# Kernel optimization log

Hardware: AMD Instinct MI355X
Metric: run time of the kernel (lower is better)

Reference implementation:

```python
import jax, jax.numpy as jnp
import numpy as np

B, C, Q, E = 32, 1024, 128, 512

def setup_inputs() -> dict:
    key = jax.random.key(0)
    k1, k2, k3 = jax.random.split(key, 3)
    context = jax.random.normal(k1, (B, C, E), dtype=jnp.float32)
    question = jax.random.normal(k2, (B, Q, E), dtype=jnp.float32)
    # ws = [ws_q | ws_c | ws_m], matching cat([q, ctx, q*ctx]) order
    ws = jax.random.normal(k3, (3 * E,), dtype=jnp.float32) * (1.0 / np.sqrt(E))
    return {"context": context, "question": question, "ws": ws}

def reference(context, question, ws):
    ws_q, ws_c, ws_m = ws[:E], ws[E:2 * E], ws[2 * E:]
    # similarity[b,c,q] = ws_q.q[b,q] + ws_c.c[b,c] + ws_m.(q[b,q]*c[b,c])
    sim = (jnp.einsum('bqe,e->bq', question, ws_q)[:, None, :]
           + jnp.einsum('bce,e->bc', context, ws_c)[:, :, None]
           + jnp.einsum('bce,bqe,e->bcq', context, question, ws_m))  # (B,C,Q)
    c2q = jnp.einsum('bcq,bqe->bce', jax.nn.softmax(sim, axis=2), question)  # (B,C,E)
    q2c_w = jax.nn.softmax(jnp.max(sim, axis=2), axis=1)  # (B,C)
    q2c = jnp.einsum('bc,bce->be', q2c_w, context)[:, None, :]  # (B,1,E)
    return (c2q, q2c)
```

## Files before the change

### kernel.cpp

```cpp
#include <hip/hip_runtime.h>

#define BB 32
#define CC 1024
#define QQ 128
#define EE 512

typedef unsigned int uint32;
typedef unsigned short u16;
typedef __bf16 bf16x8 __attribute__((ext_vector_type(8)));
typedef float f32x4 __attribute__((ext_vector_type(4)));

#define QMF_OFF  (0u)
#define QTF_OFF  (4u<<20)
#define PV_OFF   (8u<<20)
#define QD_OFF   (12u<<20)
#define MT_OFF   ((12u<<20) + 16384u)
#define ST_OFF   (MT_OFF + 8192u)

__device__ __forceinline__ u16 bfc(float f){
  __bf16 h = (__bf16)f;
  return __builtin_bit_cast(u16, h);
}
__device__ __forceinline__ float bf2f(uint32 lo16){
  return __builtin_bit_cast(float, lo16 << 16);
}

__global__ __launch_bounds__(256) void k_prep_qm(const float* __restrict__ q,
                                                 const float* __restrict__ ws,
                                                 unsigned char* __restrict__ wsp){
  const int b = blockIdx.x >> 2, et = blockIdx.x & 3, e0 = et*128;
  __shared__ u16 tile[128*136];
  const int tid = threadIdx.x;
  #pragma unroll
  for (int i=0;i<16;i++){
    int id = tid + i*256;
    int qi = id >> 5;
    int el = (id & 31) << 2;
    float4 v = *(const float4*)(q + (size_t)(b*QQ+qi)*EE + e0 + el);
    float4 m = *(const float4*)(ws + 2*EE + e0 + el);
    float4 c = *(const float4*)(ws +   EE + e0 + el);
    ushort4 u; u.x = bfc(v.x*m.x + c.x); u.y = bfc(v.y*m.y + c.y);
               u.z = bfc(v.z*m.z + c.z); u.w = bfc(v.w*m.w + c.w);
    *(ushort4*)&tile[qi*136 + el] = u;
  }
  __syncthreads();
  const int lane = tid & 63, wv = tid >> 6, l15 = lane & 15, l4 = lane >> 4;
  uint4* qmf = (uint4*)(wsp + QMF_OFF);
  #pragma unroll
  for (int i=0;i<8;i++){
    int f = wv*8 + i;
    int kl = f >> 3, nf = f & 7;
    uint4 u = *(const uint4*)&tile[(nf*16 + l15)*136 + kl*32 + l4*8];
    qmf[(size_t)((b*16 + et*4 + kl)*8 + nf)*64 + lane] = u;
  }
}

__global__ __launch_bounds__(256) void k_prep_qt(const float* __restrict__ q,
                                                 unsigned char* __restrict__ wsp){
  const int b = blockIdx.x >> 2, et = blockIdx.x & 3, e0 = et*128;
  __shared__ u16 tile[128*136];
  const int tid = threadIdx.x;
  #pragma unroll
  for (int i=0;i<16;i++){
    int id = tid + i*256;
    int qi = id >> 5;
    int el = (id & 31) << 2;
    float4 v = *(const float4*)(q + (size_t)(b*QQ+qi)*EE + e0 + el);
    ushort4 u; u.x = bfc(v.x); u.y = bfc(v.y); u.z = bfc(v.z); u.w = bfc(v.w);
    *(ushort4*)&tile[qi*136 + el] = u;
  }
  __syncthreads();
  const int lane = tid & 63, wv = tid >> 6, l15 = lane & 15, l4 = lane >> 4;
  uint4* qtf = (uint4*)(wsp + QTF_OFF);
  #pragma unroll
  for (int i=0;i<8;i++){
    int f = wv*8 + i;
    int ks2 = f >> 3, nl = f & 7, ne = et*8 + nl;
    uint32 x[4];
    #pragma unroll
    for (int p=0;p<4;p++){
      u16 t0 = tile[(ks2*32 + l4*8 + 2*p    )*136 + nl*16 + l15];
      u16 t1 = tile[(ks2*32 + l4*8 + 2*p + 1)*136 + nl*16 + l15];
      x[p] = (uint32)t0 | ((uint32)t1 << 16);
    }
    uint4 u; u.x = x[0]; u.y = x[1]; u.z = x[2]; u.w = x[3];
    qtf[(size_t)((b*4 + ks2)*32 + ne)*64 + lane] = u;
  }
}

__global__ __launch_bounds__(256) void k_prep_qd(const float* __restrict__ q,
                                                 const float* __restrict__ ws,
                                                 unsigned char* __restrict__ wsp){
  const int row = blockIdx.x*4 + (threadIdx.x >> 6);
  const int lane = threadIdx.x & 63;
  const float4* qr = (const float4*)(q + (size_t)row*EE) + lane*2;
  const float4* wq = (const float4*)ws + lane*2;
  float4 v0 = qr[0], v1 = qr[1], a0 = wq[0], a1 = wq[1];
  float dot = v0.x*a0.x + v0.y*a0.y + v0.z*a0.z + v0.w*a0.w
            + v1.x*a1.x + v1.y*a1.y + v1.z*a1.z + v1.w*a1.w;
  #pragma unroll
  for (int off=1; off<64; off<<=1) dot += __shfl_xor(dot, off);
  if (lane == 0) ((float*)(wsp + QD_OFF))[row] = dot;
}

__global__ __attribute__((amdgpu_flat_work_group_size(512, 512)))
           __attribute__((amdgpu_waves_per_eu(4, 4)))
void k_main(const float* __restrict__ ctx,
            unsigned char* __restrict__ wsp,
            float* __restrict__ out){
  __shared__ __align__(16) unsigned char tile[65536];
  __shared__ __align__(16) float mx_s[64*8];
  __shared__ __align__(16) float sm_s[64*8];
  __shared__ float wrow_s[4][16];

  const int bid = blockIdx.x;
  const int sw  = (bid & 7)*64 + (bid >> 3);
  const int b   = sw >> 4;
  const int t   = sw & 15;
  const int tid = threadIdx.x;
  const int lane = tid & 63;
  const int w    = tid >> 6;
  const int l15  = lane & 15;
  const int l4   = lane >> 4;
  const int rg   = w >> 1;
  const int eh   = w & 1;

  const float4* cb4 = (const float4*)(ctx + (size_t)(b*CC + t*64)*EE);
  {
    float4 v[16];
    #pragma unroll
    for (int i=0;i<16;i++) v[i] = cb4[i*512 + tid];
    const int colb = (tid & 127)*8;
    #pragma unroll
    for (int i=0;i<16;i++){
      int row = i*4 + (tid >> 7);
      uint2 u;
      u.x = (uint32)bfc(v[i].x) | ((uint32)bfc(v[i].y) << 16);
      u.y = (uint32)bfc(v[i].z) | ((uint32)bfc(v[i].w) << 16);
      *(uint2*)(tile + row*1024 + (colb ^ ((row & 7) << 4))) = u;
    }
  }
  const uint4* qmf4 = (const uint4*)(wsp + QMF_OFF);
  bf16x8 a[16];
  #pragma unroll
  for (int ks=0; ks<16; ks++)
    a[ks] = __builtin_bit_cast(bf16x8, qmf4[(size_t)((b*16 + ks)*8 + w)*64 + lane]);
  const float4 qdv = *(const float4*)((const float*)(wsp + QD_OFF) + b*QQ + w*16 + l4*4);
  __syncthreads();

  f32x4 acc[4];
  #pragma unroll
  for (int cc=0;cc<4;cc++) acc[cc] = (f32x4){0.f,0.f,0.f,0.f};
  #pragma unroll
  for (int ks=0; ks<16; ks++){
    #pragma unroll
    for (int cc=0; cc<4; cc++){
      const int row = cc*16 + l15;
      bf16x8 bf = __builtin_bit_cast(bf16x8,
        *(const uint4*)(tile + row*1024 + ((ks*64 + l4*16) ^ ((row & 7) << 4))));
      acc[cc] = __builtin_amdgcn_mfma_f32_16x16x32_bf16(a[ks], bf, acc[cc], 0, 0, 0);
    }
  }
  __syncthreads();

  {
    float pm[4], ps[4];
    #pragma unroll
    for (int cc=0; cc<4; cc++){
      float m = -3.0e38f, s = 0.f;
      u16 hb[4];
      #pragma unroll
      for (int r=0;r<4;r++){
        float vv = acc[cc][r] + qdv[r];
        vv = fminf(vv, 80.f);
        m = fmaxf(m, vv);
        u16 h = bfc(__expf(vv));
        hb[r] = h;
        s += bf2f(h);
      }
      uint2 u; u.x = (uint32)hb[0] | ((uint32)hb[1]<<16);
               u.y = (uint32)hb[2] | ((uint32)hb[3]<<16);
      *(uint2*)(tile + (cc*4 + (w>>1))*1024 + (((w&1)*2 + (l4>>1))*16 + l15)*16 + (l4&1)*8) = u;
      m = fmaxf(m, __shfl_xor(m, 16)); m = fmaxf(m, __shfl_xor(m, 32));
      s += __shfl_xor(s, 16);          s += __shfl_xor(s, 32);
      pm[cc] = m; ps[cc] = s;
    }
    if (l4 == 0){
      #pragma unroll
      for (int cc=0; cc<4; cc++){
        mx_s[(cc*16 + l15)*8 + w] = pm[cc];
        sm_s[(cc*16 + l15)*8 + w] = ps[cc];
      }
    }
  }
  __syncthreads();

  float rden[4];
  #pragma unroll
  for (int r=0;r<4;r++){
    const int c = rg*16 + l4*4 + r;
    f32x4 s0 = *(const f32x4*)&sm_s[c*8];
    f32x4 s1 = *(const f32x4*)&sm_s[c*8 + 4];
    rden[r] = 1.f/(s0[0]+s0[1]+s0[2]+s0[3]+s1[0]+s1[1]+s1[2]+s1[3]);
  }

  if (eh == 0){
    float mf[4];
    #pragma unroll
    for (int r=0;r<4;r++){
      const int c = rg*16 + l4*4 + r;
      f32x4 m0 = *(const f32x4*)&mx_s[c*8];
      f32x4 m1 = *(const f32x4*)&mx_s[c*8 + 4];
      mf[r] = fmaxf(fmaxf(fmaxf(m0[0],m0[1]), fmaxf(m0[2],m0[3])),
                    fmaxf(fmaxf(m1[0],m1[1]), fmaxf(m1[2],m1[3])));
    }
    float m16 = fmaxf(fmaxf(mf[0],mf[1]), fmaxf(mf[2],mf[3]));
    m16 = fmaxf(m16, __shfl_xor(m16, 16));
    m16 = fmaxf(m16, __shfl_xor(m16, 32));
    float wr[4], s16 = 0.f;
    #pragma unroll
    for (int r=0;r<4;r++){ wr[r] = __expf(mf[r] - m16); s16 += wr[r]; }
    s16 += __shfl_xor(s16, 16);
    s16 += __shfl_xor(s16, 32);
    if (l15 == 0){
      #pragma unroll
      for (int r=0;r<4;r++) wrow_s[rg][l4*4 + r] = wr[r];
    }
    if (lane == 0){
      ((float*)(wsp + MT_OFF))[b*64 + t*4 + rg] = m16;
      ((float*)(wsp + ST_OFF))[b*64 + t*4 + rg] = s16;
    }
  }

  bf16x8 pa[4];
  #pragma unroll
  for (int k2=0;k2<4;k2++)
    pa[k2] = __builtin_bit_cast(bf16x8, *(const uint4*)(tile + (rg*4 + k2)*1024 + lane*16));

  unsigned char* qstage = tile + 16384;
  const unsigned char* qtfb = wsp + QTF_OFF + (size_t)b*131072;
  auto dma = [&](int p){
    #pragma unroll
    for (int j=0;j<2;j++){
      const int f = w*2 + j;
      const int ks2 = f >> 2, nl = f & 3;
      const unsigned char* g = qtfb + (size_t)(ks2*32 + p*4 + nl)*1024 + lane*16;
      __builtin_amdgcn_global_load_lds(
        (const __attribute__((address_space(1))) uint32*)g,
        (__attribute__((address_space(3))) uint32*)(qstage + (p&1)*16384 + f*1024),
        16, 0, 0);
    }
  };
  dma(0);
  __syncthreads();

  float* ob = out + (size_t)(b*CC + t*64 + rg*16)*EE;
  #pragma unroll
  for (int p=0; p<8; p++){
    if (p < 7) dma(p+1);
    const unsigned char* qs = qstage + (p&1)*16384;
    f32x4 ac0 = (f32x4){0.f,0.f,0.f,0.f};
    f32x4 ac1 = (f32x4){0.f,0.f,0.f,0.f};
    #pragma unroll
    for (int k2=0;k2<4;k2++){
      bf16x8 b0 = __builtin_bit_cast(bf16x8, *(const uint4*)(qs + (k2*4 + eh*2 + 0)*1024 + lane*16));
      bf16x8 b1 = __builtin_bit_cast(bf16x8, *(const uint4*)(qs + (k2*4 + eh*2 + 1)*1024 + lane*16));
      ac0 = __builtin_amdgcn_mfma_f32_16x16x32_bf16(pa[k2], b0, ac0, 0, 0, 0);
      ac1 = __builtin_amdgcn_mfma_f32_16x16x32_bf16(pa[k2], b1, ac1, 0, 0, 0);
    }
    #pragma unroll
    for (int r=0;r<4;r++){
      ob[(size_t)(l4*4 + r)*EE + p*64 + eh*32 +  0 + l15] = ac0[r]*rden[r];
      ob[(size_t)(l4*4 + r)*EE + p*64 + eh*32 + 16 + l15] = ac1[r]*rden[r];
    }
    __syncthreads();
  }

  {
    const float4* cq = (const float4*)(ctx + (size_t)(b*CC + t*64 + rg*16)*EE + eh*256) + lane;
    float4 a4; a4.x = 0.f; a4.y = 0.f; a4.z = 0.f; a4.w = 0.f;
    #pragma unroll
    for (int rr=0; rr<16; rr++){
      float wv = wrow_s[rg][rr];
      float4 g = cq[(size_t)rr*128];
      a4.x = fmaf(wv, g.x, a4.x); a4.y = fmaf(wv, g.y, a4.y);
      a4.z = fmaf(wv, g.z, a4.z); a4.w = fmaf(wv, g.w, a4.w);
    }
    float* pv = (float*)(wsp + PV_OFF) + (size_t)(b*64 + t*4 + rg)*EE + eh*256 + lane*4;
    *(float4*)pv = a4;
  }
}

__global__ __launch_bounds__(256) void k_fin(unsigned char* __restrict__ wsp,
                                             float* __restrict__ out){
  const int b = blockIdx.x;
  __shared__ float sc_s[64];
  const int tid = threadIdx.x;
  if (tid < 64){
    float Mg = ((const float*)(wsp + MT_OFF))[b*64 + tid];
    float Sg = ((const float*)(wsp + ST_OFF))[b*64 + tid];
    float M = Mg;
    #pragma unroll
    for (int off=1; off<64; off<<=1) M = fmaxf(M, __shfl_xor(M, off));
    float ev = __expf(Mg - M);
    float ds = ev * Sg;
    #pragma unroll
    for (int off=1; off<64; off<<=1) ds += __shfl_xor(ds, off);
    sc_s[tid] = ev / ds;
  }
  __syncthreads();
  const float* pv = (const float*)(wsp + PV_OFF) + (size_t)b*64*EE;
  float a0 = 0.f, a1 = 0.f;
  #pragma unroll 8
  for (int g=0; g<64; g++){
    float s = sc_s[g];
    a0 = fmaf(s, pv[g*EE + tid],       a0);
    a1 = fmaf(s, pv[g*EE + tid + 256], a1);
  }
  size_t base = (size_t)BB*CC*EE + (size_t)b*EE;
  out[base + tid]       = a0;
  out[base + tid + 256] = a1;
}

extern "C" void kernel_launch(void* const* d_in, const int* in_sizes, int n_in,
                              void* d_out, int out_size, void* d_ws, size_t ws_size,
                              hipStream_t stream){
  const float* ctx = (const float*)d_in[0];
  const float* q   = (const float*)d_in[1];
  const float* ws  = (const float*)d_in[2];
  float* out = (float*)d_out;
  unsigned char* wsp = (unsigned char*)d_ws;

  k_prep_qm<<<dim3(BB*4),    dim3(256), 0, stream>>>(q, ws, wsp);
  k_prep_qt<<<dim3(BB*4),    dim3(256), 0, stream>>>(q, wsp);
  k_prep_qd<<<dim3(BB*QQ/4), dim3(256), 0, stream>>>(q, ws, wsp);
  k_main   <<<dim3(512),     dim3(512), 0, stream>>>(ctx, wsp, out);
  k_fin    <<<dim3(BB),      dim3(256), 0, stream>>>(wsp, out);
}
```

Before: 58.58 us.

## Merge prep kernels and process two context tiles per main block

The three question-preprocessing kernels are fused into one that emits the bf16 QM and QT fragments plus per-slice partial q·ws_q dots in a single pass over the question. The main kernel now handles two 64-row context tiles per block with double-buffered LDS (128KB). It prefetches the second tile's context during the first tile's GEMM and softmax, and reuses each staged QT chunk for both tiles in the c2q GEMM. This removes two launches and halves QT staging traffic. In exchange the grid drops to 256 blocks, occupancy falls (waves_per_eu 2, larger LDS), and register pressure rises.

```diff
diff --git a/kernel.cpp b/kernel.cpp
--- a/kernel.cpp
+++ b/kernel.cpp
@@ -13,8 +13,8 @@
 #define QMF_OFF  (0u)
 #define QTF_OFF  (4u<<20)
 #define PV_OFF   (8u<<20)
-#define QD_OFF   (12u<<20)
-#define MT_OFF   ((12u<<20) + 16384u)
+#define QDP_OFF  (12u<<20)
+#define MT_OFF   ((12u<<20) + 65536u)
 #define ST_OFF   (MT_OFF + 8192u)
 
 __device__ __forceinline__ u16 bfc(float f){
@@ -25,53 +25,44 @@
   return __builtin_bit_cast(float, lo16 << 16);
 }
 
-__global__ __launch_bounds__(256) void k_prep_qm(const float* __restrict__ q,
-                                                 const float* __restrict__ ws,
-                                                 unsigned char* __restrict__ wsp){
+__global__ __launch_bounds__(256) void k_prep(const float* __restrict__ q,
+                                              const float* __restrict__ ws,
+                                              unsigned char* __restrict__ wsp){
   const int b = blockIdx.x >> 2, et = blockIdx.x & 3, e0 = et*128;
-  __shared__ u16 tile[128*136];
+  __shared__ u16 tm[128*136];
+  __shared__ u16 tt[128*136];
   const int tid = threadIdx.x;
+  float* qdp = (float*)(wsp + QDP_OFF) + (size_t)(b*4 + et)*128;
   #pragma unroll
   for (int i=0;i<16;i++){
     int id = tid + i*256;
     int qi = id >> 5;
     int el = (id & 31) << 2;
     float4 v = *(const float4*)(q + (size_t)(b*QQ+qi)*EE + e0 + el);
-    float4 m = *(const float4*)(ws + 2*EE + e0 + el);
-    float4 c = *(const float4*)(ws +   EE + e0 + el);
-    ushort4 u; u.x = bfc(v.x*m.x + c.x); u.y = bfc(v.y*m.y + c.y);
-               u.z = bfc(v.z*m.z + c.z); u.w = bfc(v.w*m.w + c.w);
-    *(ushort4*)&tile[qi*136 + el] = u;
+    float4 a = *(const float4*)(ws +          e0 + el);
+    float4 c = *(const float4*)(ws +   EE +   e0 + el);
+    float4 m = *(const float4*)(ws + 2*EE +   e0 + el);
+    ushort4 um; um.x = bfc(v.x*m.x + c.x); um.y = bfc(v.y*m.y + c.y);
+                um.z = bfc(v.z*m.z + c.z); um.w = bfc(v.w*m.w + c.w);
+    *(ushort4*)&tm[qi*136 + el] = um;
+    ushort4 ut; ut.x = bfc(v.x); ut.y = bfc(v.y); ut.z = bfc(v.z); ut.w = bfc(v.w);
+    *(ushort4*)&tt[qi*136 + el] = ut;
+    float d = v.x*a.x + v.y*a.y + v.z*a.z + v.w*a.w;
+    d += __shfl_xor(d,1); d += __shfl_xor(d,2); d += __shfl_xor(d,4);
+    d += __shfl_xor(d,8); d += __shfl_xor(d,16);
+    if ((tid & 31) == 0) qdp[qi] = d;
   }
   __syncthreads();
   const int lane = tid & 63, wv = tid >> 6, l15 = lane & 15, l4 = lane >> 4;
   uint4* qmf = (uint4*)(wsp + QMF_OFF);
+  uint4* qtf = (uint4*)(wsp + QTF_OFF);
   #pragma unroll
   for (int i=0;i<8;i++){
     int f = wv*8 + i;
     int kl = f >> 3, nf = f & 7;
-    uint4 u = *(const uint4*)&tile[(nf*16 + l15)*136 + kl*32 + l4*8];
+    uint4 u = *(const uint4*)&tm[(nf*16 + l15)*136 + kl*32 + l4*8];
     qmf[(size_t)((b*16 + et*4 + kl)*8 + nf)*64 + lane] = u;
   }
-}
-
-__global__ __launch_bounds__(256) void k_prep_qt(const float* __restrict__ q,
-                                                 unsigned char* __restrict__ wsp){
-  const int b = blockIdx.x >> 2, et = blockIdx.x & 3, e0 = et*128;
-  __shared__ u16 tile[128*136];
-  const int tid = threadIdx.x;
-  #pragma unroll
-  for (int i=0;i<16;i++){
-    int id = tid + i*256;
-    int qi = id >> 5;
-    int el = (id & 31) << 2;
-    float4 v = *(const float4*)(q + (size_t)(b*QQ+qi)*EE + e0 + el);
-    ushort4 u; u.x = bfc(v.x); u.y = bfc(v.y); u.z = bfc(v.z); u.w = bfc(v.w);
-    *(ushort4*)&tile[qi*136 + el] = u;
-  }
-  __syncthreads();
-  const int lane = tid & 63, wv = tid >> 6, l15 = lane & 15, l4 = lane >> 4;
-  uint4* qtf = (uint4*)(wsp + QTF_OFF);
   #pragma unroll
   for (int i=0;i<8;i++){
     int f = wv*8 + i;
@@ -79,8 +70,8 @@
     uint32 x[4];
     #pragma unroll
     for (int p=0;p<4;p++){
-      u16 t0 = tile[(ks2*32 + l4*8 + 2*p    )*136 + nl*16 + l15];
-      u16 t1 = tile[(ks2*32 + l4*8 + 2*p + 1)*136 + nl*16 + l15];
+      u16 t0 = tt[(ks2*32 + l4*8 + 2*p    )*136 + nl*16 + l15];
+      u16 t1 = tt[(ks2*32 + l4*8 + 2*p + 1)*136 + nl*16 + l15];
       x[p] = (uint32)t0 | ((uint32)t1 << 16);
     }
     uint4 u; u.x = x[0]; u.y = x[1]; u.z = x[2]; u.w = x[3];
@@ -88,35 +79,21 @@
   }
 }
 
-__global__ __launch_bounds__(256) void k_prep_qd(const float* __restrict__ q,
-                                                 const float* __restrict__ ws,
-                                                 unsigned char* __restrict__ wsp){
-  const int row = blockIdx.x*4 + (threadIdx.x >> 6);
-  const int lane = threadIdx.x & 63;
-  const float4* qr = (const float4*)(q + (size_t)row*EE) + lane*2;
-  const float4* wq = (const float4*)ws + lane*2;
-  float4 v0 = qr[0], v1 = qr[1], a0 = wq[0], a1 = wq[1];
-  float dot = v0.x*a0.x + v0.y*a0.y + v0.z*a0.z + v0.w*a0.w
-            + v1.x*a1.x + v1.y*a1.y + v1.z*a1.z + v1.w*a1.w;
-  #pragma unroll
-  for (int off=1; off<64; off<<=1) dot += __shfl_xor(dot, off);
-  if (lane == 0) ((float*)(wsp + QD_OFF))[row] = dot;
-}
-
 __global__ __attribute__((amdgpu_flat_work_group_size(512, 512)))
-           __attribute__((amdgpu_waves_per_eu(4, 4)))
+           __attribute__((amdgpu_waves_per_eu(2)))
 void k_main(const float* __restrict__ ctx,
             unsigned char* __restrict__ wsp,
             float* __restrict__ out){
-  __shared__ __align__(16) unsigned char tile[65536];
-  __shared__ __align__(16) float mx_s[64*8];
-  __shared__ __align__(16) float sm_s[64*8];
-  __shared__ float wrow_s[4][16];
+  __shared__ __align__(16) unsigned char buf[2][65536];
+  __shared__ __align__(16) float mxA[2][64*8];
+  __shared__ __align__(16) float smA[2][64*8];
+  __shared__ float wrowA[2][4][16];
 
   const int bid = blockIdx.x;
-  const int sw  = (bid & 7)*64 + (bid >> 3);
-  const int b   = sw >> 4;
-  const int t   = sw & 15;
+  const int sw  = (bid & 7)*32 + (bid >> 3);
+  const int b   = sw >> 3;
+  const int pr  = sw & 7;
+  const int t0  = pr*2, t1 = pr*2 + 1;
   const int tid = threadIdx.x;
   const int lane = tid & 63;
   const int w    = tid >> 6;
@@ -125,53 +102,71 @@
   const int rg   = w >> 1;
   const int eh   = w & 1;
 
-  const float4* cb4 = (const float4*)(ctx + (size_t)(b*CC + t*64)*EE);
+  const float4* cb0 = (const float4*)(ctx + (size_t)(b*CC + t0*64)*EE);
+  const float4* cb1 = (const float4*)(ctx + (size_t)(b*CC + t1*64)*EE);
+  float4 v[16];
+  #pragma unroll
+  for (int i=0;i<16;i++) v[i] = cb0[i*512 + tid];
+
+  const uint4* qmf4 = (const uint4*)(wsp + QMF_OFF);
+  bf16x8 a[16];
+  #pragma unroll
+  for (int ks=0; ks<16; ks++)
+    a[ks] = __builtin_bit_cast(bf16x8, qmf4[(size_t)((b*16 + ks)*8 + w)*64 + lane]);
+  float qdv[4];
   {
-    float4 v[16];
-    #pragma unroll
-    for (int i=0;i<16;i++) v[i] = cb4[i*512 + tid];
-    const int colb = (tid & 127)*8;
+    const float* qdp = (const float*)(wsp + QDP_OFF) + (size_t)b*512;
+    #pragma unroll
+    for (int r=0;r<4;r++){
+      const int qi = w*16 + l4*4 + r;
+      qdv[r] = qdp[qi] + qdp[128+qi] + qdp[256+qi] + qdp[384+qi];
+    }
+  }
+
+  const int colb = (tid & 127)*8;
+  auto stage_write = [&](unsigned char* dst){
     #pragma unroll
     for (int i=0;i<16;i++){
       int row = i*4 + (tid >> 7);
       uint2 u;
       u.x = (uint32)bfc(v[i].x) | ((uint32)bfc(v[i].y) << 16);
       u.y = (uint32)bfc(v[i].z) | ((uint32)bfc(v[i].w) << 16);
-      *(uint2*)(tile + row*1024 + (colb ^ ((row & 7) << 4))) = u;
-    }
-  }
-  const uint4* qmf4 = (const uint4*)(wsp + QMF_OFF);
-  bf16x8 a[16];
-  #pragma unroll
-  for (int ks=0; ks<16; ks++)
-    a[ks] = __builtin_bit_cast(bf16x8, qmf4[(size_t)((b*16 + ks)*8 + w)*64 + lane]);
-  const float4 qdv = *(const float4*)((const float*)(wsp + QD_OFF) + b*QQ + w*16 + l4*4);
-  __syncthreads();
-
+      *(uint2*)(dst + row*1024 + (colb ^ ((row & 7) << 4))) = u;
+    }
+  };
+
+  stage_write(buf[0]);
+  __syncthreads();
+
+  #pragma unroll
+  for (int i=0;i<16;i++) v[i] = cb1[i*512 + tid];
+
+  auto gemm1 = [&](const unsigned char* bp, f32x4* acc){
+    #pragma unroll
+    for (int cc=0;cc<4;cc++) acc[cc] = (f32x4){0.f,0.f,0.f,0.f};
+    #pragma unroll
+    for (int ks=0; ks<16; ks++){
+      #pragma unroll
+      for (int cc=0; cc<4; cc++){
+        const int row = cc*16 + l15;
+        bf16x8 bf = __builtin_bit_cast(bf16x8,
+          *(const uint4*)(bp + row*1024 + ((ks*64 + l4*16) ^ ((row & 7) << 4))));
+        acc[cc] = __builtin_amdgcn_mfma_f32_16x16x32_bf16(a[ks], bf, acc[cc], 0, 0, 0);
+      }
+    }
+  };
   f32x4 acc[4];
-  #pragma unroll
-  for (int cc=0;cc<4;cc++) acc[cc] = (f32x4){0.f,0.f,0.f,0.f};
-  #pragma unroll
-  for (int ks=0; ks<16; ks++){
-    #pragma unroll
-    for (int cc=0; cc<4; cc++){
-      const int row = cc*16 + l15;
-      bf16x8 bf = __builtin_bit_cast(bf16x8,
-        *(const uint4*)(tile + row*1024 + ((ks*64 + l4*16) ^ ((row & 7) << 4))));
-      acc[cc] = __builtin_amdgcn_mfma_f32_16x16x32_bf16(a[ks], bf, acc[cc], 0, 0, 0);
-    }
-  }
-  __syncthreads();
-
-  {
-    float pm[4], ps[4];
+  gemm1(buf[0], acc);
+  __syncthreads();
+
+  auto softmax = [&](int ti, f32x4* ac){
     #pragma unroll
     for (int cc=0; cc<4; cc++){
       float m = -3.0e38f, s = 0.f;
       u16 hb[4];
       #pragma unroll
       for (int r=0;r<4;r++){
-        float vv = acc[cc][r] + qdv[r];
+        float vv = ac[cc][r] + qdv[r];
         vv = fminf(vv, 80.f);
         m = fmaxf(m, vv);
         u16 h = bfc(__expf(vv));
@@ -180,37 +175,36 @@
       }
       uint2 u; u.x = (uint32)hb[0] | ((uint32)hb[1]<<16);
                u.y = (uint32)hb[2] | ((uint32)hb[3]<<16);
-      *(uint2*)(tile + (cc*4 + (w>>1))*1024 + (((w&1)*2 + (l4>>1))*16 + l15)*16 + (l4&1)*8) = u;
+      *(uint2*)(buf[ti] + (cc*4 + (w>>1))*1024 + (((w&1)*2 + (l4>>1))*16 + l15)*16 + (l4&1)*8) = u;
       m = fmaxf(m, __shfl_xor(m, 16)); m = fmaxf(m, __shfl_xor(m, 32));
       s += __shfl_xor(s, 16);          s += __shfl_xor(s, 32);
-      pm[cc] = m; ps[cc] = s;
-    }
-    if (l4 == 0){
-      #pragma unroll
-      for (int cc=0; cc<4; cc++){
-        mx_s[(cc*16 + l15)*8 + w] = pm[cc];
-        sm_s[(cc*16 + l15)*8 + w] = ps[cc];
+      if (l4 == 0){
+        mxA[ti][(cc*16 + l15)*8 + w] = m;
+        smA[ti][(cc*16 + l15)*8 + w] = s;
       }
     }
-  }
-  __syncthreads();
-
-  float rden[4];
-  #pragma unroll
-  for (int r=0;r<4;r++){
-    const int c = rg*16 + l4*4 + r;
-    f32x4 s0 = *(const f32x4*)&sm_s[c*8];
-    f32x4 s1 = *(const f32x4*)&sm_s[c*8 + 4];
-    rden[r] = 1.f/(s0[0]+s0[1]+s0[2]+s0[3]+s1[0]+s1[1]+s1[2]+s1[3]);
-  }
-
-  if (eh == 0){
-    float mf[4];
+  };
+  softmax(0, acc);
+  stage_write(buf[1]);
+  __syncthreads();
+
+  auto rden_of = [&](int ti, float* rd){
     #pragma unroll
     for (int r=0;r<4;r++){
       const int c = rg*16 + l4*4 + r;
-      f32x4 m0 = *(const f32x4*)&mx_s[c*8];
-      f32x4 m1 = *(const f32x4*)&mx_s[c*8 + 4];
+      f32x4 s0 = *(const f32x4*)&smA[ti][c*8];
+      f32x4 s1 = *(const f32x4*)&smA[ti][c*8 + 4];
+      rd[r] = 1.f/(s0[0]+s0[1]+s0[2]+s0[3]+s1[0]+s1[1]+s1[2]+s1[3]);
+    }
+  };
+  auto q2c_stats = [&](int ti, int tglob){
+    if (eh != 0) return;
+    float mf[4];
+    #pragma unroll
+    for (int r=0;r<4;r++){
+      const int c = rg*16 + l4*4 + r;
+      f32x4 m0 = *(const f32x4*)&mxA[ti][c*8];
+      f32x4 m1 = *(const f32x4*)&mxA[ti][c*8 + 4];
       mf[r] = fmaxf(fmaxf(fmaxf(m0[0],m0[1]), fmaxf(m0[2],m0[3])),
                     fmaxf(fmaxf(m1[0],m1[1]), fmaxf(m1[2],m1[3])));
     }
@@ -224,20 +218,23 @@
     s16 += __shfl_xor(s16, 32);
     if (l15 == 0){
       #pragma unroll
-      for (int r=0;r<4;r++) wrow_s[rg][l4*4 + r] = wr[r];
+      for (int r=0;r<4;r++) wrowA[ti][rg][l4*4 + r] = wr[r];
     }
     if (lane == 0){
-      ((float*)(wsp + MT_OFF))[b*64 + t*4 + rg] = m16;
-      ((float*)(wsp + ST_OFF))[b*64 + t*4 + rg] = s16;
-    }
-  }
-
-  bf16x8 pa[4];
+      ((float*)(wsp + MT_OFF))[b*64 + tglob*4 + rg] = m16;
+      ((float*)(wsp + ST_OFF))[b*64 + tglob*4 + rg] = s16;
+    }
+  };
+
+  float rden0[4], rden1[4];
+  rden_of(0, rden0);
+  q2c_stats(0, t0);
+  bf16x8 pa0[4], pa1[4];
   #pragma unroll
   for (int k2=0;k2<4;k2++)
-    pa[k2] = __builtin_bit_cast(bf16x8, *(const uint4*)(tile + (rg*4 + k2)*1024 + lane*16));
-
-  unsigned char* qstage = tile + 16384;
+    pa0[k2] = __builtin_bit_cast(bf16x8, *(const uint4*)(buf[0] + (rg*4 + k2)*1024 + lane*16));
+
+  unsigned char* qstage = buf[0] + 16384;
   const unsigned char* qtfb = wsp + QTF_OFF + (size_t)b*131072;
   auto dma = [&](int p){
     #pragma unroll
@@ -252,41 +249,60 @@
     }
   };
   dma(0);
-  __syncthreads();
-
-  float* ob = out + (size_t)(b*CC + t*64 + rg*16)*EE;
+
+  gemm1(buf[1], acc);
+  __syncthreads();
+  softmax(1, acc);
+  __syncthreads();
+  rden_of(1, rden1);
+  q2c_stats(1, t1);
+  #pragma unroll
+  for (int k2=0;k2<4;k2++)
+    pa1[k2] = __builtin_bit_cast(bf16x8, *(const uint4*)(buf[1] + (rg*4 + k2)*1024 + lane*16));
+
+  float* ob0 = out + (size_t)(b*CC + t0*64 + rg*16)*EE;
+  float* ob1 = out + (size_t)(b*CC + t1*64 + rg*16)*EE;
   #pragma unroll
   for (int p=0; p<8; p++){
     if (p < 7) dma(p+1);
     const unsigned char* qs = qstage + (p&1)*16384;
-    f32x4 ac0 = (f32x4){0.f,0.f,0.f,0.f};
-    f32x4 ac1 = (f32x4){0.f,0.f,0.f,0.f};
+    f32x4 A0 = (f32x4){0.f,0.f,0.f,0.f};
+    f32x4 A1 = (f32x4){0.f,0.f,0.f,0.f};
+    f32x4 B0 = (f32x4){0.f,0.f,0.f,0.f};
+    f32x4 B1 = (f32x4){0.f,0.f,0.f,0.f};
     #pragma unroll
     for (int k2=0;k2<4;k2++){
       bf16x8 b0 = __builtin_bit_cast(bf16x8, *(const uint4*)(qs + (k2*4 + eh*2 + 0)*1024 + lane*16));
       bf16x8 b1 = __builtin_bit_cast(bf16x8, *(const uint4*)(qs + (k2*4 + eh*2 + 1)*1024 + lane*16));
-      ac0 = __builtin_amdgcn_mfma_f32_16x16x32_bf16(pa[k2], b0, ac0, 0, 0, 0);
-      ac1 = __builtin_amdgcn_mfma_f32_16x16x32_bf16(pa[k2], b1, ac1, 0, 0, 0);
+      A0 = __builtin_amdgcn_mfma_f32_16x16x32_bf16(pa0[k2], b0, A0, 0, 0, 0);
+      A1 = __builtin_amdgcn_mfma_f32_16x16x32_bf16(pa0[k2], b1, A1, 0, 0, 0);
+      B0 = __builtin_amdgcn_mfma_f32_16x16x32_bf16(pa1[k2], b0, B0, 0, 0, 0);
+      B1 = __builtin_amdgcn_mfma_f32_16x16x32_bf16(pa1[k2], b1, B1, 0, 0, 0);
     }
     #pragma unroll
     for (int r=0;r<4;r++){
-      ob[(size_t)(l4*4 + r)*EE + p*64 + eh*32 +  0 + l15] = ac0[r]*rden[r];
-      ob[(size_t)(l4*4 + r)*EE + p*64 + eh*32 + 16 + l15] = ac1[r]*rden[r];
+      const size_t ro = (size_t)(l4*4 + r)*EE + p*64 + eh*32;
+      ob0[ro +      l15] = A0[r]*rden0[r];
+      ob0[ro + 16 + l15] = A1[r]*rden0[r];
+      ob1[ro +      l15] = B0[r]*rden1[r];
+      ob1[ro + 16 + l15] = B1[r]*rden1[r];
     }
     __syncthreads();
   }
 
-  {
-    const float4* cq = (const float4*)(ctx + (size_t)(b*CC + t*64 + rg*16)*EE + eh*256) + lane;
+  #pragma unroll
+  for (int ti=0; ti<2; ti++){
+    const int tg = ti ? t1 : t0;
+    const float4* cq = (const float4*)(ctx + (size_t)(b*CC + tg*64 + rg*16)*EE + eh*256) + lane;
     float4 a4; a4.x = 0.f; a4.y = 0.f; a4.z = 0.f; a4.w = 0.f;
     #pragma unroll
     for (int rr=0; rr<16; rr++){
-      float wv = wrow_s[rg][rr];
+      float wv = wrowA[ti][rg][rr];
       float4 g = cq[(size_t)rr*128];
       a4.x = fmaf(wv, g.x, a4.x); a4.y = fmaf(wv, g.y, a4.y);
       a4.z = fmaf(wv, g.z, a4.z); a4.w = fmaf(wv, g.w, a4.w);
     }
-    float* pv = (float*)(wsp + PV_OFF) + (size_t)(b*64 + t*4 + rg)*EE + eh*256 + lane*4;
+    float* pv = (float*)(wsp + PV_OFF) + (size_t)(b*64 + tg*4 + rg)*EE + eh*256 + lane*4;
     *(float4*)pv = a4;
   }
 }
@@ -331,9 +347,7 @@
   float* out = (float*)d_out;
   unsigned char* wsp = (unsigned char*)d_ws;
 
-  k_prep_qm<<<dim3(BB*4),    dim3(256), 0, stream>>>(q, ws, wsp);
-  k_prep_qt<<<dim3(BB*4),    dim3(256), 0, stream>>>(q, wsp);
-  k_prep_qd<<<dim3(BB*QQ/4), dim3(256), 0, stream>>>(q, ws, wsp);
-  k_main   <<<dim3(512),     dim3(512), 0, stream>>>(ctx, wsp, out);
-  k_fin    <<<dim3(BB),      dim3(256), 0, stream>>>(wsp, out);
-}
+  k_prep<<<dim3(BB*4), dim3(256), 0, stream>>>(q, ws, wsp);
+  k_main<<<dim3(256),  dim3(512), 0, stream>>>(ctx, wsp, out);
+  k_fin <<<dim3(BB),   dim3(256), 0, stream>>>(wsp, out);
+}
```

Measured after the change: 59.22 us. Within noise of the previous version (+1.1%).
